# Performance work log

Measured on AMD Instinct MI355X. Metric: run time of the kernel, lower is better.

Reference implementation:

```python
import jax, jax.numpy as jnp
import numpy as np


def _binop(ei, ej):
    # diagonal linear recurrence combine: (a_i, b_i) * (a_j, b_j) -> (a_j*a_i, a_j*b_i + b_j)
    ai, bi = ei
    aj, bj = ej
    return aj * ai, aj * bi + bj


def setup_inputs() -> dict:
    key = jax.random.key(0)
    ks = jax.random.split(key, 9)
    B_, T, D_in, D_out, N = 16, 2048, 512, 512, 512
    inp = {
        "input": jax.random.normal(ks[0], (B_, T, D_in), dtype=jnp.float32),
        "D": jax.random.normal(ks[1], (D_out, D_in), dtype=jnp.float32) / np.sqrt(D_in),
        "nu_log": jax.random.normal(ks[2], (N,), dtype=jnp.float32),
        "theta_log": jax.random.normal(ks[3], (N,), dtype=jnp.float32),
        "gamma_log": jax.random.normal(ks[4], (N,), dtype=jnp.float32),
        "B_re": jax.random.normal(ks[5], (N, D_in), dtype=jnp.float32) / np.sqrt(2 * D_in),
        "B_im": jax.random.normal(ks[6], (N, D_in), dtype=jnp.float32) / np.sqrt(2 * D_in),
        "C_re": jax.random.normal(ks[7], (D_out, N), dtype=jnp.float32) / np.sqrt(N),
        "C_im": jax.random.normal(ks[8], (D_out, N), dtype=jnp.float32) / np.sqrt(N),
    }
    return inp


def reference(input, D, nu_log, theta_log, gamma_log, B_re, B_im, C_re, C_im):
    # ss_params
    lam_abs = jnp.exp(-jnp.exp(nu_log))                      # [N]
    lam_phase = jnp.exp(theta_log)                           # [N]
    lam = lam_abs * (jnp.cos(lam_phase) + 1j * jnp.sin(lam_phase))  # complex [N]
    gamma = jnp.exp(gamma_log)                               # [N]
    Bc = (B_re + 1j * B_im) * gamma[:, None]                 # [N, D_in]
    Cc = C_re + 1j * C_im                                    # [D_out, N]

    # input projection: Bu_elements [batch, T, N] (complex)
    Bu = input.astype(Bc.dtype) @ Bc.T
    lam_el = jnp.broadcast_to(lam, Bu.shape)

    # parallel associative scan over time axis (initial state is zero)
    _, states = jax.lax.associative_scan(_binop, (lam_el, Bu), axis=1)

    # readout
    y = jnp.real(states @ Cc.T) + input @ D.T                # [batch, T, D_out]
    return y
```

## Files before the change

kernel.cpp:

```cpp
#include <hip/hip_runtime.h>
#include <hip/hip_fp16.h>

typedef _Float16 f16;
typedef __attribute__((ext_vector_type(8))) _Float16 f16x8;
typedef __attribute__((ext_vector_type(2))) _Float16 f16x2;
typedef __attribute__((ext_vector_type(4))) float f32x4;

#define B_SZ 16
#define T_SZ 2048
#define DIN 512
#define DOUT 512
#define N_SZ 512
#define M_SZ (B_SZ * T_SZ)
#define LCHUNK 64
#define NCHUNK 32

__device__ __forceinline__ void gload_lds16(const void* g, void* l) {
  __builtin_amdgcn_global_load_lds(
      (const __attribute__((address_space(1))) void*)g,
      (__attribute__((address_space(3))) void*)l, 16, 0, 0);
}


__global__ void prep_all(const float* __restrict__ nu_log,
                         const float* __restrict__ theta_log,
                         const float* __restrict__ gamma_log,
                         const float* __restrict__ B_re, const float* __restrict__ B_im,
                         const float* __restrict__ C_re, const float* __restrict__ C_im,
                         const float* __restrict__ Dm, const float* __restrict__ input,
                         float2* __restrict__ lam2, float2* __restrict__ lamL2,
                         float2* __restrict__ lamp,
                         f16* __restrict__ W1, f16* __restrict__ W2,
                         f16* __restrict__ inp16) {
  int b = blockIdx.x;
  if (b < 2) {
    int n = b * 256 + threadIdx.x;
    float nu = expf(nu_log[n]);
    float ph = expf(theta_log[n]);
    float la = expf(-nu);
    lam2[n] = make_float2(la * cosf(ph), la * sinf(ph));
    float laL = expf(-nu * (float)LCHUNK);
    float phL = ph * (float)LCHUNK;
    lamL2[n] = make_float2(laL * cosf(phL), laL * sinf(phL));
  } else if (b < 4) {
    int n = (b - 2) * 256 + threadIdx.x;
    float nu = expf(nu_log[n]);
    float ph = expf(theta_log[n]);
    float la = expf(-nu);
    float2 l1 = make_float2(la * cosf(ph), la * sinf(ph));
    float2 cur = l1;
    for (int j = 0; j < LCHUNK; ++j) {
      lamp[(size_t)j * 512 + n] = cur;
      float nre = cur.x * l1.x - cur.y * l1.y;
      cur.y = cur.x * l1.y + cur.y * l1.x;
      cur.x = nre;
    }
  } else if (b < 4 + 2048) {
    int tid = (b - 4) * 256 + threadIdx.x;
    int np = tid >> 9;
    int d = tid & 511;
    int n = np >> 1;
    float g = expf(gamma_log[n]);
    const float* src = (np & 1) ? B_im : B_re;
    W1[(size_t)np * 512 + d] = (f16)(src[(size_t)n * 512 + d] * g);
  } else if (b < 4 + 2048 + 3072) {
    int tid = (b - 2052) * 256 + threadIdx.x;
    int j = tid / 1536;
    int k = tid - j * 1536;
    float v;
    if (k < 1024) {
      int n = k >> 1;
      v = (k & 1) ? -C_im[(size_t)j * 512 + n] : C_re[(size_t)j * 512 + n];
    } else {
      v = Dm[(size_t)j * 512 + (k - 1024)];
    }
    W2[(size_t)j * 1536 + k] = (f16)v;
  } else {
    int tid = (b - 5124) * 256 + threadIdx.x;
    int m = tid >> 6;
    int d0 = (tid & 63) << 3;
    const float4* p = (const float4*)(input + (size_t)m * DIN + d0);
    float4 a = p[0], c = p[1];
    f16x8 h;
    h[0] = (f16)a.x; h[1] = (f16)a.y; h[2] = (f16)a.z; h[3] = (f16)a.w;
    h[4] = (f16)c.x; h[5] = (f16)c.y; h[6] = (f16)c.z; h[7] = (f16)c.w;
    *(f16x8*)(inp16 + (size_t)m * 512 + d0) = h;
  }
}


__global__ void scan_b(const float2* __restrict__ S, const float2* __restrict__ lamL2,
                       float2* __restrict__ Carry) {
  int tid = blockIdx.x * 256 + threadIdx.x;
  int n = tid & 511;
  int b = tid >> 9;
  float2 lL = lamL2[n];
  float cre = 0.f, cim = 0.f;
  for (int c = 0; c < NCHUNK; ++c) {
    size_t idx = (size_t)(b * NCHUNK + c) * 512 + n;
    Carry[idx] = make_float2(cre, cim);
    float2 s = S[idx];
    float nre = lL.x * cre - lL.y * cim + s.x;
    cim = lL.x * cim + lL.y * cre + s.y;
    cre = nre;
  }
}


__global__ __launch_bounds__(512, 2) void gemm_fuse(
    const f16* __restrict__ A, const f16* __restrict__ Bm,
    const float2* __restrict__ lam2, unsigned* __restrict__ sloc_out,
    float2* __restrict__ Svec) {
  extern __shared__ f16 smem[];
  f16* sA = smem;
  f16* sB = smem + 2 * 16384;
  const int lda = 512, ldb = 512, K = 512, nxt = 4;

  const int tid = threadIdx.x;
  const int lane = tid & 63;
  const int wid = tid >> 6;
  const int wr = wid >> 2;
  const int wc = wid & 3;
  const int fr = lane & 15;
  const int fg = lane >> 4;
  const int xr = fr & 7;

  const int nwg = gridDim.x;
  const int id = blockIdx.x;
  const int swz = (id & 7) * (nwg >> 3) + (id >> 3);
  const int m0 = (swz / nxt) * 256;
  const int n0 = (swz % nxt) * 256;

  const int srow = tid >> 3;
  const int scol = ((tid & 7) ^ (srow & 7)) * 8;
  const int sdst = wid * 512;
  const int NT = K >> 6;

  f32x4 acc[8][4];
#pragma unroll
  for (int i = 0; i < 8; ++i)
#pragma unroll
    for (int j = 0; j < 4; ++j) acc[i][j] = f32x4{0.f, 0.f, 0.f, 0.f};

  const int ar0 = wr * 128;
  const int bc0 = wc * 64;

  auto stage = [&](int t) {
    const int b = t & 1;
    f16* dA = sA + b * 16384 + sdst;
    f16* dB = sB + b * 16384 + sdst;
    const f16* gA = A + (size_t)(m0 + srow) * lda + t * 64 + scol;
    const f16* gB = Bm + (size_t)(n0 + srow) * ldb + t * 64 + scol;
    gload_lds16(gA, dA);
    gload_lds16(gA + (size_t)64 * lda, dA + 4096);
    gload_lds16(gA + (size_t)128 * lda, dA + 8192);
    gload_lds16(gA + (size_t)192 * lda, dA + 12288);
    gload_lds16(gB, dB);
    gload_lds16(gB + (size_t)64 * ldb, dB + 4096);
    gload_lds16(gB + (size_t)128 * ldb, dB + 8192);
    gload_lds16(gB + (size_t)192 * ldb, dB + 12288);
  };

  auto barrier = [&]() {
    __builtin_amdgcn_sched_barrier(0);
    __builtin_amdgcn_s_barrier();
    __builtin_amdgcn_sched_barrier(0);
  };

  stage(0);
  asm volatile("s_waitcnt vmcnt(0)" ::: "memory");
  barrier();

  f16x8 bf[4][2];
  for (int t = 0; t < NT; ++t) {
    const int b = t & 1;
    const f16* bA = sA + b * 16384;
    const f16* bB = sB + b * 16384;
    if (t + 1 < NT) stage(t + 1);
#pragma unroll
    for (int h = 0; h < 4; ++h) {
      if (h == 0) {
#pragma unroll
        for (int nrep = 0; nrep < 4; ++nrep)
#pragma unroll
          for (int ks = 0; ks < 2; ++ks) {
            int row = bc0 + nrep * 16 + fr;
            bf[nrep][ks] =
                *(const f16x8*)(bB + row * 64 + (((ks * 4 + fg) ^ xr) * 8));
          }
      }
      f16x8 af[2][2];
#pragma unroll
      for (int mi = 0; mi < 2; ++mi)
#pragma unroll
        for (int ks = 0; ks < 2; ++ks) {
          int row = ar0 + (h * 2 + mi) * 16 + fr;
          af[mi][ks] =
              *(const f16x8*)(bA + row * 64 + (((ks * 4 + fg) ^ xr) * 8));
        }
      __builtin_amdgcn_s_setprio(1);
#pragma unroll
      for (int mi = 0; mi < 2; ++mi)
#pragma unroll
        for (int nrep = 0; nrep < 4; ++nrep)
#pragma unroll
          for (int ks = 0; ks < 2; ++ks)
            acc[h * 2 + mi][nrep] = __builtin_amdgcn_mfma_f32_16x16x32_f16(
                af[mi][ks], bf[nrep][ks], acc[h * 2 + mi][nrep], 0, 0, 0);
      __builtin_amdgcn_s_setprio(0);
      if (h == 3 && t + 1 < NT)
        asm volatile("s_waitcnt vmcnt(0)" ::: "memory");
      barrier();
    }
  }

  f16* reg = smem + wid * 8192;
#pragma unroll
  for (int mi = 0; mi < 8; ++mi)
#pragma unroll
    for (int ni = 0; ni < 4; ++ni)
#pragma unroll
      for (int r = 0; r < 4; ++r)
        reg[(mi * 16 + fg * 4 + r) * 64 + ni * 16 + fr] = (f16)acc[mi][ni][r];
  __syncthreads();
  const int half = lane >> 5;
  const int nc = lane & 31;
  const int n = ((n0 + wc * 64) >> 1) + nc;
  const float2 l2 = lam2[n];
  const f16* col = smem + wid * 8192 + (half * 64) * 64 + 2 * nc;
  const int mbase = m0 + wr * 128 + half * 64;
  unsigned* sp = sloc_out + (size_t)mbase * 512 + n;
  float sre = 0.f, sim = 0.f;
#pragma unroll 1
  for (int j0 = 0; j0 < 64; j0 += 8) {
    f16x2 u[8];
#pragma unroll
    for (int q = 0; q < 8; ++q) u[q] = *(const f16x2*)(col + (j0 + q) * 64);
#pragma unroll
    for (int q = 0; q < 8; ++q) {
      float nre = l2.x * sre - l2.y * sim + (float)u[q].x;
      sim = l2.x * sim + l2.y * sre + (float)u[q].y;
      sre = nre;
      f16x2 o;
      o.x = (f16)sre;
      o.y = (f16)sim;
      sp[(size_t)(j0 + q) * 512] = __builtin_bit_cast(unsigned, o);
    }
  }
  Svec[(size_t)((m0 >> 11) * NCHUNK + ((mbase >> 6) & (NCHUNK - 1))) * 512 + n] =
      make_float2(sre, sim);
}


__global__ __launch_bounds__(256, 2) void gemm_ro(
    const f16* __restrict__ inp16, const f16* __restrict__ W2,
    float* __restrict__ C,
    const unsigned* __restrict__ sloc, const float2* __restrict__ lamp,
    const float2* __restrict__ Carry) {
  extern __shared__ f16 smem[];
  const int ldb = 1536, ldc = 512, NT = 24;

  const int tid = threadIdx.x;
  const int lane = tid & 63;
  const int wid = tid >> 6;
  const int wr = wid >> 1;
  const int wc = wid & 1;
  const int fr = lane & 15;
  const int fg = lane >> 4;
  const int xr = fr & 7;

  const int nwg = gridDim.x;
  const int id = blockIdx.x;
  const int swz = (id & 7) * (nwg >> 3) + (id >> 3);
  const int m0 = (swz >> 2) * 128;
  const int n0 = (swz & 3) * 128;

  const int srow = tid >> 3;
  const int slot = (tid & 7) ^ (srow & 7);
  const int scol = slot * 8;
  const int sdst = wid * 512;

  f32x4 acc[4][4];
#pragma unroll
  for (int i = 0; i < 4; ++i)
#pragma unroll
    for (int j = 0; j < 4; ++j) acc[i][j] = f32x4{0.f, 0.f, 0.f, 0.f};

  auto stageB = [&](int t) {
    f16* dB = smem + (t & 1) * 16384 + 8192 + sdst;
    const f16* gB = W2 + (size_t)(n0 + srow) * ldb + t * 64 + scol;
#pragma unroll
    for (int i = 0; i < 4; ++i)
      gload_lds16(gB + (size_t)(32 * i) * ldb, dB + i * 2048);
  };
  auto stageA_g = [&](int t) {
    f16* dA = smem + (t & 1) * 16384 + sdst;
    const f16* gA = inp16 + (size_t)(m0 + srow) * 512 + (t - 16) * 64 + scol;
#pragma unroll
    for (int i = 0; i < 4; ++i)
      gload_lds16(gA + (size_t)(32 * i) * 512, dA + i * 2048);
  };

  uint4 sl[4];
  float2 lpq[2][4];
  float2 crq[2][4];

  auto cstage_issue = [&](int t) {
    const int nq = t * 32 + slot * 4;
    const unsigned* sp = sloc + (size_t)(m0 + srow) * 512 + nq;
#pragma unroll
    for (int i = 0; i < 4; ++i)
      sl[i] = *(const uint4*)(sp + (size_t)(32 * i) * 512);
#pragma unroll
    for (int p = 0; p < 2; ++p) {
      const float2* lpp = lamp + (size_t)(srow + 32 * p) * 512 + nq;
      const float2* crp = Carry + (size_t)((m0 >> 6) + p) * 512 + nq;
#pragma unroll
      for (int q = 0; q < 4; ++q) {
        lpq[p][q] = lpp[q];
        crq[p][q] = crp[q];
      }
    }
  };
  auto cstage_finish = [&](int t) {
    f16* dA = smem + (t & 1) * 16384;
#pragma unroll
    for (int i = 0; i < 4; ++i) {
      unsigned u4[4] = {sl[i].x, sl[i].y, sl[i].z, sl[i].w};
      f16x8 o;
#pragma unroll
      for (int q = 0; q < 4; ++q) {
        f16x2 u = __builtin_bit_cast(f16x2, u4[q]);
        float lx = lpq[i & 1][q].x, ly = lpq[i & 1][q].y;
        float cx = crq[i >> 1][q].x, cy = crq[i >> 1][q].y;
        o[2 * q] = (f16)((float)u.x + lx * cx - ly * cy);
        o[2 * q + 1] = (f16)((float)u.y + lx * cy + ly * cx);
      }
      *(f16x8*)(dA + (srow + 32 * i) * 64 + (tid & 7) * 8) = o;
    }
  };

  auto stage_issue = [&](int t) {
    stageB(t);
    if (t < 16)
      cstage_issue(t);
    else
      stageA_g(t);
  };

  stage_issue(0);
  cstage_finish(0);
  asm volatile("s_waitcnt vmcnt(0) lgkmcnt(0)" ::: "memory");
  __builtin_amdgcn_sched_barrier(0);
  __builtin_amdgcn_s_barrier();
  __builtin_amdgcn_sched_barrier(0);

  for (int t = 0; t < NT; ++t) {
    const f16* bA = smem + (t & 1) * 16384;
    const f16* bB = bA + 8192;
    if (t + 1 < NT) stage_issue(t + 1);

    f16x8 af[4][2], bf[4][2];
#pragma unroll
    for (int mi = 0; mi < 4; ++mi)
#pragma unroll
      for (int ks = 0; ks < 2; ++ks)
        af[mi][ks] = *(const f16x8*)(bA + (wr * 64 + mi * 16 + fr) * 64 +
                                     (((ks * 4 + fg) ^ xr) * 8));
#pragma unroll
    for (int ni = 0; ni < 4; ++ni)
#pragma unroll
      for (int ks = 0; ks < 2; ++ks)
        bf[ni][ks] = *(const f16x8*)(bB + (wc * 64 + ni * 16 + fr) * 64 +
                                     (((ks * 4 + fg) ^ xr) * 8));
    __builtin_amdgcn_s_setprio(1);
#pragma unroll
    for (int mi = 0; mi < 4; ++mi)
#pragma unroll
      for (int ni = 0; ni < 4; ++ni)
#pragma unroll
        for (int ks = 0; ks < 2; ++ks)
          acc[mi][ni] = __builtin_amdgcn_mfma_f32_16x16x32_f16(
              af[mi][ks], bf[ni][ks], acc[mi][ni], 0, 0, 0);
    __builtin_amdgcn_s_setprio(0);
    if (t + 1 < NT && t + 1 < 16) cstage_finish(t + 1);
    asm volatile("s_waitcnt vmcnt(0) lgkmcnt(0)" ::: "memory");
    __builtin_amdgcn_sched_barrier(0);
    __builtin_amdgcn_s_barrier();
    __builtin_amdgcn_sched_barrier(0);
  }

#pragma unroll
  for (int mi = 0; mi < 4; ++mi) {
    int rbase = m0 + wr * 64 + mi * 16 + fg * 4;
#pragma unroll
    for (int ni = 0; ni < 4; ++ni) {
      int col = n0 + wc * 64 + ni * 16 + fr;
#pragma unroll
      for (int r = 0; r < 4; ++r)
        C[(size_t)(rbase + r) * ldc + col] = acc[mi][ni][r];
    }
  }
}


extern "C" void kernel_launch(void* const* d_in, const int* in_sizes, int n_in,
                              void* d_out, int out_size, void* d_ws, size_t ws_size,
                              hipStream_t stream) {
  const float* input = (const float*)d_in[0];
  const float* Dmat = (const float*)d_in[1];
  const float* nu_log = (const float*)d_in[2];
  const float* theta_log = (const float*)d_in[3];
  const float* gamma_log = (const float*)d_in[4];
  const float* B_re = (const float*)d_in[5];
  const float* B_im = (const float*)d_in[6];
  const float* C_re = (const float*)d_in[7];
  const float* C_im = (const float*)d_in[8];
  float* y = (float*)d_out;

  char* ws = (char*)d_ws;
  size_t off = 0;
  auto alloc = [&](size_t bytes) {
    void* p = ws + off;
    off = (off + bytes + 255) & ~(size_t)255;
    return p;
  };
  float2* lam2 = (float2*)alloc(N_SZ * sizeof(float2));
  float2* lamL2 = (float2*)alloc(N_SZ * sizeof(float2));
  float2* lamp = (float2*)alloc((size_t)LCHUNK * N_SZ * sizeof(float2));
  f16* W1 = (f16*)alloc((size_t)2 * N_SZ * DIN * 2);
  f16* W2 = (f16*)alloc((size_t)DOUT * 1536 * 2);
  f16* inp16 = (f16*)alloc((size_t)M_SZ * DIN * 2);
  unsigned* sloc = (unsigned*)alloc((size_t)M_SZ * N_SZ * 4);
  float2* S = (float2*)alloc((size_t)B_SZ * NCHUNK * N_SZ * sizeof(float2));
  float2* Carry = (float2*)alloc((size_t)B_SZ * NCHUNK * N_SZ * sizeof(float2));

  {
    hipFuncSetAttribute((const void*)gemm_fuse,
                        hipFuncAttributeMaxDynamicSharedMemorySize, 131072);
    hipFuncSetAttribute((const void*)gemm_ro,
                        hipFuncAttributeMaxDynamicSharedMemorySize, 65536);
  }

  prep_all<<<13316, 256, 0, stream>>>(nu_log, theta_log, gamma_log, B_re, B_im,
                                      C_re, C_im, Dmat, input, lam2, lamL2, lamp,
                                      W1, W2, inp16);

  gemm_fuse<<<512, 512, 131072, stream>>>(inp16, W1, lam2, sloc, S);

  scan_b<<<(B_SZ * N_SZ) / 256, 256, 0, stream>>>(S, lamL2, Carry);

  gemm_ro<<<1024, 256, 65536, stream>>>(inp16, W2, y, sloc, lamp, Carry);
}
```

Measured before the change: 150.4 us.

## Enlarge readout GEMM tile to 256x256 with 8 waves and split K-step into phases

```diff
diff --git a/kernel.cpp b/kernel.cpp
--- a/kernel.cpp
+++ b/kernel.cpp
@@ -252,19 +252,21 @@
 }
 
 
-__global__ __launch_bounds__(256, 2) void gemm_ro(
+__global__ __launch_bounds__(512, 2) void gemm_ro(
     const f16* __restrict__ inp16, const f16* __restrict__ W2,
     float* __restrict__ C,
     const unsigned* __restrict__ sloc, const float2* __restrict__ lamp,
     const float2* __restrict__ Carry) {
   extern __shared__ f16 smem[];
-  const int ldb = 1536, ldc = 512, NT = 24;
+  f16* sA = smem;
+  f16* sB = smem + 2 * 16384;
+  const int ldb = 1536, ldc = 512, NT = 24, nxt = 2;
 
   const int tid = threadIdx.x;
   const int lane = tid & 63;
   const int wid = tid >> 6;
-  const int wr = wid >> 1;
-  const int wc = wid & 1;
+  const int wr = wid >> 2;
+  const int wc = wid & 3;
   const int fr = lane & 15;
   const int fg = lane >> 4;
   const int xr = fr & 7;
@@ -272,58 +274,59 @@
   const int nwg = gridDim.x;
   const int id = blockIdx.x;
   const int swz = (id & 7) * (nwg >> 3) + (id >> 3);
-  const int m0 = (swz >> 2) * 128;
-  const int n0 = (swz & 3) * 128;
+  const int m0 = (swz / nxt) * 256;
+  const int n0 = (swz % nxt) * 256;
 
   const int srow = tid >> 3;
-  const int slot = (tid & 7) ^ (srow & 7);
-  const int scol = slot * 8;
+  const int scol = ((tid & 7) ^ (srow & 7)) * 8;
   const int sdst = wid * 512;
 
-  f32x4 acc[4][4];
-#pragma unroll
-  for (int i = 0; i < 4; ++i)
+  f32x4 acc[8][4];
+#pragma unroll
+  for (int i = 0; i < 8; ++i)
 #pragma unroll
     for (int j = 0; j < 4; ++j) acc[i][j] = f32x4{0.f, 0.f, 0.f, 0.f};
 
+  const int ar0 = wr * 128;
+  const int bc0 = wc * 64;
+
   auto stageB = [&](int t) {
-    f16* dB = smem + (t & 1) * 16384 + 8192 + sdst;
+    f16* dB = sB + (t & 1) * 16384 + sdst;
     const f16* gB = W2 + (size_t)(n0 + srow) * ldb + t * 64 + scol;
-#pragma unroll
-    for (int i = 0; i < 4; ++i)
-      gload_lds16(gB + (size_t)(32 * i) * ldb, dB + i * 2048);
+    gload_lds16(gB, dB);
+    gload_lds16(gB + (size_t)64 * ldb, dB + 4096);
+    gload_lds16(gB + (size_t)128 * ldb, dB + 8192);
+    gload_lds16(gB + (size_t)192 * ldb, dB + 12288);
   };
   auto stageA_g = [&](int t) {
-    f16* dA = smem + (t & 1) * 16384 + sdst;
+    f16* dA = sA + (t & 1) * 16384 + sdst;
     const f16* gA = inp16 + (size_t)(m0 + srow) * 512 + (t - 16) * 64 + scol;
-#pragma unroll
-    for (int i = 0; i < 4; ++i)
-      gload_lds16(gA + (size_t)(32 * i) * 512, dA + i * 2048);
+    gload_lds16(gA, dA);
+    gload_lds16(gA + (size_t)64 * 512, dA + 4096);
+    gload_lds16(gA + (size_t)128 * 512, dA + 8192);
+    gload_lds16(gA + (size_t)192 * 512, dA + 12288);
   };
 
   uint4 sl[4];
-  float2 lpq[2][4];
-  float2 crq[2][4];
+  float2 lpq[4];
+  float2 crq[4][4];
 
   auto cstage_issue = [&](int t) {
-    const int nq = t * 32 + slot * 4;
+    const int nq = t * 32 + (scol >> 1);
     const unsigned* sp = sloc + (size_t)(m0 + srow) * 512 + nq;
-#pragma unroll
-    for (int i = 0; i < 4; ++i)
-      sl[i] = *(const uint4*)(sp + (size_t)(32 * i) * 512);
-#pragma unroll
-    for (int p = 0; p < 2; ++p) {
-      const float2* lpp = lamp + (size_t)(srow + 32 * p) * 512 + nq;
-      const float2* crp = Carry + (size_t)((m0 >> 6) + p) * 512 + nq;
-#pragma unroll
-      for (int q = 0; q < 4; ++q) {
-        lpq[p][q] = lpp[q];
-        crq[p][q] = crp[q];
-      }
+    const float2* lpp = lamp + (size_t)srow * 512 + nq;
+    const float2* crp = Carry + (size_t)(m0 >> 6) * 512 + nq;
+#pragma unroll
+    for (int q = 0; q < 4; ++q) lpq[q] = lpp[q];
+#pragma unroll
+    for (int i = 0; i < 4; ++i) {
+      sl[i] = *(const uint4*)(sp + (size_t)i * 64 * 512);
+#pragma unroll
+      for (int q = 0; q < 4; ++q) crq[i][q] = crp[(size_t)i * 512 + q];
     }
   };
   auto cstage_finish = [&](int t) {
-    f16* dA = smem + (t & 1) * 16384;
+    f16* dst = sA + (t & 1) * 16384 + tid * 8;
 #pragma unroll
     for (int i = 0; i < 4; ++i) {
       unsigned u4[4] = {sl[i].x, sl[i].y, sl[i].z, sl[i].w};
@@ -331,12 +334,12 @@
 #pragma unroll
       for (int q = 0; q < 4; ++q) {
         f16x2 u = __builtin_bit_cast(f16x2, u4[q]);
-        float lx = lpq[i & 1][q].x, ly = lpq[i & 1][q].y;
-        float cx = crq[i >> 1][q].x, cy = crq[i >> 1][q].y;
+        float lx = lpq[q].x, ly = lpq[q].y;
+        float cx = crq[i][q].x, cy = crq[i][q].y;
         o[2 * q] = (f16)((float)u.x + lx * cx - ly * cy);
         o[2 * q + 1] = (f16)((float)u.y + lx * cy + ly * cx);
       }
-      *(f16x8*)(dA + (srow + 32 * i) * 64 + (tid & 7) * 8) = o;
+      *(f16x8*)(dst + i * 4096) = o;
     }
   };
 
@@ -348,54 +351,67 @@
       stageA_g(t);
   };
 
+  auto barrier = [&]() {
+    __builtin_amdgcn_sched_barrier(0);
+    __builtin_amdgcn_s_barrier();
+    __builtin_amdgcn_sched_barrier(0);
+  };
+
   stage_issue(0);
   cstage_finish(0);
   asm volatile("s_waitcnt vmcnt(0) lgkmcnt(0)" ::: "memory");
-  __builtin_amdgcn_sched_barrier(0);
-  __builtin_amdgcn_s_barrier();
-  __builtin_amdgcn_sched_barrier(0);
-
+  barrier();
+
+  f16x8 bf[4][2];
   for (int t = 0; t < NT; ++t) {
-    const f16* bA = smem + (t & 1) * 16384;
-    const f16* bB = bA + 8192;
+    const int b = t & 1;
+    const f16* bA = sA + b * 16384;
+    const f16* bB = sB + b * 16384;
     if (t + 1 < NT) stage_issue(t + 1);
-
-    f16x8 af[4][2], bf[4][2];
-#pragma unroll
-    for (int mi = 0; mi < 4; ++mi)
-#pragma unroll
-      for (int ks = 0; ks < 2; ++ks)
-        af[mi][ks] = *(const f16x8*)(bA + (wr * 64 + mi * 16 + fr) * 64 +
-                                     (((ks * 4 + fg) ^ xr) * 8));
-#pragma unroll
-    for (int ni = 0; ni < 4; ++ni)
-#pragma unroll
-      for (int ks = 0; ks < 2; ++ks)
-        bf[ni][ks] = *(const f16x8*)(bB + (wc * 64 + ni * 16 + fr) * 64 +
-                                     (((ks * 4 + fg) ^ xr) * 8));
-    __builtin_amdgcn_s_setprio(1);
-#pragma unroll
-    for (int mi = 0; mi < 4; ++mi)
-#pragma unroll
-      for (int ni = 0; ni < 4; ++ni)
-#pragma unroll
-        for (int ks = 0; ks < 2; ++ks)
-          acc[mi][ni] = __builtin_amdgcn_mfma_f32_16x16x32_f16(
-              af[mi][ks], bf[ni][ks], acc[mi][ni], 0, 0, 0);
-    __builtin_amdgcn_s_setprio(0);
-    if (t + 1 < NT && t + 1 < 16) cstage_finish(t + 1);
-    asm volatile("s_waitcnt vmcnt(0) lgkmcnt(0)" ::: "memory");
-    __builtin_amdgcn_sched_barrier(0);
-    __builtin_amdgcn_s_barrier();
-    __builtin_amdgcn_sched_barrier(0);
-  }
-
-#pragma unroll
-  for (int mi = 0; mi < 4; ++mi) {
-    int rbase = m0 + wr * 64 + mi * 16 + fg * 4;
+#pragma unroll
+    for (int h = 0; h < 4; ++h) {
+      if (h == 0) {
+#pragma unroll
+        for (int nrep = 0; nrep < 4; ++nrep)
+#pragma unroll
+          for (int ks = 0; ks < 2; ++ks) {
+            int row = bc0 + nrep * 16 + fr;
+            bf[nrep][ks] =
+                *(const f16x8*)(bB + row * 64 + (((ks * 4 + fg) ^ xr) * 8));
+          }
+      }
+      f16x8 af[2][2];
+#pragma unroll
+      for (int mi = 0; mi < 2; ++mi)
+#pragma unroll
+        for (int ks = 0; ks < 2; ++ks) {
+          int row = ar0 + (h * 2 + mi) * 16 + fr;
+          af[mi][ks] =
+              *(const f16x8*)(bA + row * 64 + (((ks * 4 + fg) ^ xr) * 8));
+        }
+      if (h == 3 && t + 1 < NT && t + 1 < 16) cstage_finish(t + 1);
+      __builtin_amdgcn_s_setprio(1);
+#pragma unroll
+      for (int mi = 0; mi < 2; ++mi)
+#pragma unroll
+        for (int nrep = 0; nrep < 4; ++nrep)
+#pragma unroll
+          for (int ks = 0; ks < 2; ++ks)
+            acc[h * 2 + mi][nrep] = __builtin_amdgcn_mfma_f32_16x16x32_f16(
+                af[mi][ks], bf[nrep][ks], acc[h * 2 + mi][nrep], 0, 0, 0);
+      __builtin_amdgcn_s_setprio(0);
+      if (h == 3 && t + 1 < NT)
+        asm volatile("s_waitcnt vmcnt(0) lgkmcnt(0)" ::: "memory");
+      barrier();
+    }
+  }
+
+#pragma unroll
+  for (int mi = 0; mi < 8; ++mi) {
+    int rbase = m0 + ar0 + mi * 16 + fg * 4;
 #pragma unroll
     for (int ni = 0; ni < 4; ++ni) {
-      int col = n0 + wc * 64 + ni * 16 + fr;
+      int col = n0 + bc0 + ni * 16 + fr;
 #pragma unroll
       for (int r = 0; r < 4; ++r)
         C[(size_t)(rbase + r) * ldc + col] = acc[mi][ni][r];
@@ -439,7 +455,7 @@
     hipFuncSetAttribute((const void*)gemm_fuse,
                         hipFuncAttributeMaxDynamicSharedMemorySize, 131072);
     hipFuncSetAttribute((const void*)gemm_ro,
-                        hipFuncAttributeMaxDynamicSharedMemorySize, 65536);
+                        hipFuncAttributeMaxDynamicSharedMemorySize, 131072);
   }
 
   prep_all<<<13316, 256, 0, stream>>>(nu_log, theta_log, gamma_log, B_re, B_im,
@@ -450,5 +466,5 @@
 
   scan_b<<<(B_SZ * N_SZ) / 256, 256, 0, stream>>>(S, lamL2, Carry);
 
-  gemm_ro<<<1024, 256, 65536, stream>>>(inp16, W2, y, sloc, lamp, Carry);
-}
+  gemm_ro<<<256, 512, 131072, stream>>>(inp16, W2, y, sloc, lamp, Carry);
+}
```

After: 169.5 us. +12.7%, slower.
